# Optimization experiments

Hardware: AMD Instinct MI355X
Metric: run time of the kernel (lower is better)

Reference implementation:

```python
import jax, jax.numpy as jnp
import numpy as np

BN_EPS = 1e-5


def _edge_conv(x, W, b, gamma, beta, k):
    # x: [B, N, C_in]; W: [C_out, 2*C_in]
    inner = jnp.einsum('bnc,bmc->bnm', x, x)                 # [B,N,N]
    xx = jnp.sum(x * x, axis=-1)                             # [B,N]
    neg_dist = 2.0 * inner - xx[:, :, None] - xx[:, None, :]  # -||xi-xj||^2
    idx = jax.lax.top_k(neg_dist, k)[1]                      # [B,N,k]
    nbr = jax.vmap(lambda xb, ib: xb[ib])(x, idx)            # [B,N,k,C_in]
    ctr = x[:, :, None, :]                                   # [B,N,1,C_in]
    ef = jnp.concatenate([jnp.broadcast_to(ctr, nbr.shape), nbr - ctr], axis=-1)  # [B,N,k,2C]
    h = jnp.einsum('bnkc,oc->bnko', ef, W) + b               # 1x1 conv -> [B,N,k,C_out]
    # BatchNorm2d (training mode: biased batch stats over B,N,k)
    mean = jnp.mean(h, axis=(0, 1, 2))
    var = jnp.mean(jnp.square(h - mean), axis=(0, 1, 2))
    h = (h - mean) * jax.lax.rsqrt(var + BN_EPS) * gamma + beta
    h = jax.nn.relu(h)
    return jnp.max(h, axis=2)                                # max over k neighbors -> [B,N,C_out]


def setup_inputs() -> dict:
    key = jax.random.key(0)
    ks = jax.random.split(key, 8)
    B, N, IN = 8, 2048, 3
    dims = [64, 128, 256]
    inp = {'x': jax.random.normal(ks[0], (B, N, IN), dtype=jnp.float32)}
    prev = IN
    for i, d in enumerate(dims):
        kk = jax.random.fold_in(ks[1], i)
        inp[f'w{i+1}'] = jax.random.normal(kk, (d, 2 * prev), dtype=jnp.float32) * (1.0 / np.sqrt(2 * prev))
        inp[f'b{i+1}'] = jnp.zeros((d,), dtype=jnp.float32)
        inp[f'g{i+1}'] = jnp.ones((d,), dtype=jnp.float32)
        inp[f'be{i+1}'] = jnp.zeros((d,), dtype=jnp.float32)
        prev = d
    inp['wo'] = jax.random.normal(ks[2], (dims[-1], dims[-1]), dtype=jnp.float32) * (1.0 / np.sqrt(dims[-1]))
    inp['bo'] = jnp.zeros((dims[-1],), dtype=jnp.float32)
    inp['k'] = 20
    return inp


def reference(x, w1, b1, g1, be1, w2, b2, g2, be2, w3, b3, g3, be3, wo, bo, k):
    h = _edge_conv(x, w1, b1, g1, be1, k)
    h = _edge_conv(h, w2, b2, g2, be2, k)
    h = _edge_conv(h, w3, b3, g3, be3, k)
    h = jnp.max(h, axis=1)          # global max-pool over points -> [B, 256]
    return h @ wo.T + bo
```

## Files before the change

### kernel.cpp

```cpp
#include <hip/hip_runtime.h>
#include <cmath>

static constexpr int Bb  = 8;
static constexpr int Nn  = 2048;
static constexpr int KNB = 20;
static constexpr int NPT = Bb * Nn;
static constexpr int NTRI = 528;
#define EPSBN 1e-5f

__device__ __forceinline__ int permc(int c) { return c ^ (4 * (c >> 5)); }

__device__ __forceinline__ unsigned mkkey(float v) {
  unsigned u = __float_as_uint(v);
  return (u & 0x80000000u) ? ~u : (u | 0x80000000u);
}

__global__ __launch_bounds__(256) void row_sumsq_k(const float* __restrict__ f,
                                                   float* __restrict__ xx, int C) {
  int g = blockIdx.x * 256 + threadIdx.x;
  if (g >= NPT) return;
  const float* r = f + (size_t)g * C;
  float s = 0.f;
  if ((C & 3) == 0) {
    const float4* r4 = (const float4*)r;
    for (int j = 0; j < C / 4; ++j) {
      float4 v = r4[j];
      s += v.x * v.x + v.y * v.y + v.z * v.z + v.w * v.w;
    }
  } else {
    for (int j = 0; j < C; ++j) { float v = r[j]; s += v * v; }
  }
  xx[g] = s;
}

__global__ __launch_bounds__(256) void dist_k(const float* __restrict__ f,
                                              const float* __restrict__ xx,
                                              float* __restrict__ nd, int C) {
  __shared__ float As[16 * 68];
  __shared__ float Bs[16 * 68];
  float* Sc = As;
  int tid = threadIdx.x, tx = tid & 15, ty = tid >> 4;
  int b, p;
  if (gridDim.x == NTRI * Bb) { b = blockIdx.x & 7; p = blockIdx.x >> 3; }
  else                        { b = blockIdx.z;     p = blockIdx.x; }
  const float* fb  = f  + (size_t)b * Nn * C;
  const float* xxb = xx + (size_t)b * Nn;
  float* ndb = nd + (size_t)b * Nn * Nn;
  int rblk = 0;
  while (p >= 32 - rblk) { p -= 32 - rblk; ++rblk; }
  int rb = rblk * 64, cb = (rblk + p) * 64;
  bool diag = (rb == cb);
  int kk0 = tid & 15, rr = tid >> 4;
  float acc[4][4] = {};
  float pa[4], pb[4];
  {
    bool ok = kk0 < C;
    #pragma unroll
    for (int t = 0; t < 4; ++t) {
      int r2 = rr + 16 * t;
      pa[t] = ok ? fb[(size_t)(rb + r2) * C + kk0] : 0.f;
      pb[t] = ok ? fb[(size_t)(cb + r2) * C + kk0] : 0.f;
    }
  }
  for (int k0 = 0; k0 < C; k0 += 16) {
    __syncthreads();
    #pragma unroll
    for (int t = 0; t < 4; ++t) {
      int r2 = rr + 16 * t;
      As[kk0 * 68 + r2] = pa[t];
      Bs[kk0 * 68 + r2] = pb[t];
    }
    __syncthreads();
    if (k0 + 16 < C) {
      int k2 = k0 + 16 + kk0;
      bool ok2 = k2 < C;
      #pragma unroll
      for (int t = 0; t < 4; ++t) {
        int r2 = rr + 16 * t;
        pa[t] = ok2 ? fb[(size_t)(rb + r2) * C + k2] : 0.f;
        pb[t] = ok2 ? fb[(size_t)(cb + r2) * C + k2] : 0.f;
      }
    }
    #pragma unroll
    for (int kk = 0; kk < 16; ++kk) {
      float4 a4 = *(const float4*)&As[kk * 68 + 4 * ty];
      float4 b4 = *(const float4*)&Bs[kk * 68 + 4 * tx];
      float av[4] = {a4.x, a4.y, a4.z, a4.w};
      float bv[4] = {b4.x, b4.y, b4.z, b4.w};
      #pragma unroll
      for (int i = 0; i < 4; ++i)
        #pragma unroll
        for (int j = 0; j < 4; ++j) acc[i][j] += av[i] * bv[j];
    }
  }
  float xr[4], xc[4];
  #pragma unroll
  for (int i = 0; i < 4; ++i) xr[i] = xxb[rb + 4 * ty + i];
  #pragma unroll
  for (int j = 0; j < 4; ++j) xc[j] = xxb[cb + 4 * tx + j];
  #pragma unroll
  for (int i = 0; i < 4; ++i) {
    int grow = rb + 4 * ty + i;
    #pragma unroll
    for (int j = 0; j < 4; ++j) {
      int gcol = cb + 4 * tx + j;
      float v = 2.f * acc[i][j] - xr[i] - xc[j];
      acc[i][j] = (grow == gcol) ? 0.f : v;
    }
    *(float4*)&ndb[(size_t)grow * Nn + cb + 4 * tx] =
        make_float4(acc[i][0], acc[i][1], acc[i][2], acc[i][3]);
  }
  if (!diag) {
    int sRow = tid >> 4, c4 = tid & 15;
    #pragma unroll
    for (int h = 0; h < 4; ++h) {
      __syncthreads();
      if ((tx >> 2) == h) {
        int txl = tx & 3;
        #pragma unroll
        for (int j = 0; j < 4; ++j)
          *(float4*)&Sc[(4 * txl + j) * 68 + 4 * ty] =
              make_float4(acc[0][j], acc[1][j], acc[2][j], acc[3][j]);
      }
      __syncthreads();
      float4 v = *(const float4*)&Sc[sRow * 68 + 4 * c4];
      *(float4*)&ndb[(size_t)(cb + 16 * h + sRow) * Nn + rb + 4 * c4] = v;
    }
  }
}

__global__ __launch_bounds__(256) void topk_k(const float* __restrict__ nd,
                                              int* __restrict__ outidx) {
  __shared__ unsigned ck[Nn];
  __shared__ unsigned short ci[Nn];
  __shared__ unsigned Tw[4];
  __shared__ int s_cnt;
  int tid = threadIdx.x, lane = tid & 63;
  int n;
  if (gridDim.x == NPT) {
    int bb = blockIdx.x & 7, row = blockIdx.x >> 3;
    n = bb * Nn + row;
  } else {
    n = blockIdx.x;
  }
  const float4* rowp = (const float4*)(nd + (size_t)n * Nn);
  int* orow = outidx + (size_t)n * KNB;
  if (tid == 0) s_cnt = 0;
  float4 va = rowp[tid];
  float4 vb = rowp[tid + 256];
  unsigned k0 = mkkey(va.x), k1 = mkkey(va.y), k2 = mkkey(va.z), k3 = mkkey(va.w);
  unsigned k4 = mkkey(vb.x), k5 = mkkey(vb.y), k6 = mkkey(vb.z), k7 = mkkey(vb.w);
  unsigned t1 = k0;
  t1 = k1 > t1 ? k1 : t1; t1 = k2 > t1 ? k2 : t1; t1 = k3 > t1 ? k3 : t1;
  t1 = k4 > t1 ? k4 : t1; t1 = k5 > t1 ? k5 : t1; t1 = k6 > t1 ? k6 : t1;
  t1 = k7 > t1 ? k7 : t1;
  bool alive = true;
  unsigned wmax = 0;
  #pragma unroll
  for (int r = 0; r < 5; ++r) {
    unsigned v = alive ? t1 : 0u;
    wmax = v;
    #pragma unroll
    for (int off = 1; off < 64; off <<= 1) {
      unsigned o = (unsigned)__shfl_xor((int)wmax, off, 64);
      wmax = o > wmax ? o : wmax;
    }
    unsigned long long ball = __ballot(alive && t1 == wmax);
    int first = __ffsll((long long)ball) - 1;
    if (lane == first) alive = false;
  }
  if (lane == 0) Tw[tid >> 6] = wmax;
  __syncthreads();
  unsigned T = Tw[0];
  T = Tw[1] < T ? Tw[1] : T;
  T = Tw[2] < T ? Tw[2] : T;
  T = Tw[3] < T ? Tw[3] : T;
  int c0 = 4 * tid, c4 = 1024 + 4 * tid;
  if (k0 >= T) { int p2 = atomicAdd(&s_cnt, 1); ck[p2] = k0; ci[p2] = (unsigned short)(c0); }
  if (k1 >= T) { int p2 = atomicAdd(&s_cnt, 1); ck[p2] = k1; ci[p2] = (unsigned short)(c0 + 1); }
  if (k2 >= T) { int p2 = atomicAdd(&s_cnt, 1); ck[p2] = k2; ci[p2] = (unsigned short)(c0 + 2); }
  if (k3 >= T) { int p2 = atomicAdd(&s_cnt, 1); ck[p2] = k3; ci[p2] = (unsigned short)(c0 + 3); }
  if (k4 >= T) { int p2 = atomicAdd(&s_cnt, 1); ck[p2] = k4; ci[p2] = (unsigned short)(c4); }
  if (k5 >= T) { int p2 = atomicAdd(&s_cnt, 1); ck[p2] = k5; ci[p2] = (unsigned short)(c4 + 1); }
  if (k6 >= T) { int p2 = atomicAdd(&s_cnt, 1); ck[p2] = k6; ci[p2] = (unsigned short)(c4 + 2); }
  if (k7 >= T) { int p2 = atomicAdd(&s_cnt, 1); ck[p2] = k7; ci[p2] = (unsigned short)(c4 + 3); }
  __syncthreads();
  int nc = s_cnt;
  for (int j = tid; j < nc; j += 256) {
    unsigned kj = ck[j];
    unsigned ij = ci[j];
    int rank = 0;
    for (int i = 0; i < nc; ++i) {
      unsigned ki = ck[i];
      unsigned ii = ci[i];
      rank += (ki > kj || (ki == kj && ii < ij)) ? 1 : 0;
    }
    if (rank < KNB) orow[rank] = (int)ij;
  }
}

__global__ __launch_bounds__(256) void gemmAB_k(const float* __restrict__ X,
                                                const float* __restrict__ W,
                                                const float* __restrict__ bias,
                                                float* __restrict__ A,
                                                float* __restrict__ Bv,
                                                int COUT, int CIN) {
  __shared__ float Xs[16][132];
  __shared__ float Ws[16][132];
  int tid = threadIdx.x, tx = tid & 15, ty = tid >> 4;
  int mb = blockIdx.y * 128, cb = blockIdx.x * 128;
  int kk0 = tid & 15, rr = tid >> 4;
  int ldw = 2 * CIN;
  float acc[8][8] = {};
  for (int k0 = 0; k0 < CIN; k0 += 16) {
    int k = k0 + kk0;
    bool ok = k < CIN;
    #pragma unroll
    for (int r2 = rr; r2 < 128; r2 += 16) {
      Xs[kk0][permc(r2)] = ok ? X[(size_t)(mb + r2) * CIN + k] : 0.f;
      int c2 = cb + r2;
      const float* wr = (c2 < COUT) ? (W + (size_t)c2 * ldw)
                                    : (W + (size_t)(c2 - COUT) * ldw + CIN);
      Ws[kk0][permc(r2)] = ok ? wr[k] : 0.f;
    }
    __syncthreads();
    #pragma unroll
    for (int kk = 0; kk < 16; ++kk) {
      float4 a0 = *(const float4*)&Xs[kk][permc(8 * ty)];
      float4 a1 = *(const float4*)&Xs[kk][permc(8 * ty + 4)];
      float4 b0 = *(const float4*)&Ws[kk][permc(8 * tx)];
      float4 b1 = *(const float4*)&Ws[kk][permc(8 * tx + 4)];
      float av[8] = {a0.x, a0.y, a0.z, a0.w, a1.x, a1.y, a1.z, a1.w};
      float bv[8] = {b0.x, b0.y, b0.z, b0.w, b1.x, b1.y, b1.z, b1.w};
      #pragma unroll
      for (int i = 0; i < 8; ++i)
        #pragma unroll
        for (int j = 0; j < 8; ++j) acc[i][j] += av[i] * bv[j];
    }
    __syncthreads();
  }
  int c0 = cb + 8 * tx;
  bool isA = (c0 < COUT);
  float bb[8] = {0, 0, 0, 0, 0, 0, 0, 0};
  if (isA) {
    float4 b4a = *(const float4*)&bias[c0];
    float4 b4b = *(const float4*)&bias[c0 + 4];
    bb[0] = b4a.x; bb[1] = b4a.y; bb[2] = b4a.z; bb[3] = b4a.w;
    bb[4] = b4b.x; bb[5] = b4b.y; bb[6] = b4b.z; bb[7] = b4b.w;
  }
  float* dst = isA ? A : Bv;
  int cc = isA ? c0 : (c0 - COUT);
  #pragma unroll
  for (int i = 0; i < 8; ++i) {
    int m = mb + 8 * ty + i;
    *(float4*)&dst[(size_t)m * COUT + cc] =
        make_float4(acc[i][0] + bb[0], acc[i][1] + bb[1], acc[i][2] + bb[2], acc[i][3] + bb[3]);
    *(float4*)&dst[(size_t)m * COUT + cc + 4] =
        make_float4(acc[i][4] + bb[4], acc[i][5] + bb[5], acc[i][6] + bb[6], acc[i][7] + bb[7]);
  }
}

template <int COUT>
__global__ __launch_bounds__(256) void combine_k(const float* __restrict__ A,
                                                 const float* __restrict__ Bv,
                                                 const int* __restrict__ idx,
                                                 float* __restrict__ maxh,
                                                 float* __restrict__ minh,
                                                 float* __restrict__ gsum,
                                                 float* __restrict__ gsumsq) {
  constexpr int TPP = COUT / 4;
  constexpr int P = 256 / TPP;
  constexpr int PTS = 16;
  __shared__ float red[8][256];
  int tid = threadIdx.x;
  int p = tid / TPP, cq = tid % TPP;
  int b = blockIdx.x & 7, chunk = blockIdx.x >> 3;
  int nbase = b * Nn + chunk * PTS;
  const float4* A4 = (const float4*)A;
  const float4* B4 = (const float4*)Bv;
  float4 ts = make_float4(0, 0, 0, 0), ts2 = make_float4(0, 0, 0, 0);
  for (int it = 0; it < PTS / P; ++it) {
    int n = nbase + it * P + p;
    float4 a  = A4[(size_t)n * TPP + cq];
    float4 bc = B4[(size_t)n * TPP + cq];
    float4 base = make_float4(a.x - bc.x, a.y - bc.y, a.z - bc.z, a.w - bc.w);
    float4 mx = make_float4(-INFINITY, -INFINITY, -INFINITY, -INFINITY);
    float4 mn = make_float4(INFINITY, INFINITY, INFINITY, INFINITY);
    int gb = b * Nn;
    const int* ip = idx + (size_t)n * KNB;
    for (int k = 0; k < KNB; ++k) {
      int m = ip[k];
      float4 bn = B4[(size_t)(gb + m) * TPP + cq];
      float4 h = make_float4(base.x + bn.x, base.y + bn.y, base.z + bn.z, base.w + bn.w);
      mx.x = fmaxf(mx.x, h.x); mx.y = fmaxf(mx.y, h.y);
      mx.z = fmaxf(mx.z, h.z); mx.w = fmaxf(mx.w, h.w);
      mn.x = fminf(mn.x, h.x); mn.y = fminf(mn.y, h.y);
      mn.z = fminf(mn.z, h.z); mn.w = fminf(mn.w, h.w);
      ts.x += h.x; ts.y += h.y; ts.z += h.z; ts.w += h.w;
      ts2.x += h.x * h.x; ts2.y += h.y * h.y; ts2.z += h.z * h.z; ts2.w += h.w * h.w;
    }
    ((float4*)maxh)[(size_t)n * TPP + cq] = mx;
    ((float4*)minh)[(size_t)n * TPP + cq] = mn;
  }
  red[0][tid] = ts.x;  red[1][tid] = ts.y;  red[2][tid] = ts.z;  red[3][tid] = ts.w;
  red[4][tid] = ts2.x; red[5][tid] = ts2.y; red[6][tid] = ts2.z; red[7][tid] = ts2.w;
  __syncthreads();
  if (tid < COUT) {
    int q = tid & 3, g = tid >> 2;
    float s = 0.f, s2 = 0.f;
    for (int pp = 0; pp < P; ++pp) {
      int t2 = pp * TPP + g;
      s += red[q][t2]; s2 += red[4 + q][t2];
    }
    atomicAdd(&gsum[tid], s);
    atomicAdd(&gsumsq[tid], s2);
  }
}

__global__ void stats_k(const float* __restrict__ gsum, const float* __restrict__ gsumsq,
                        const float* __restrict__ gamma, const float* __restrict__ beta,
                        float* __restrict__ sA, float* __restrict__ sB, int COUT) {
  int c = threadIdx.x;
  if (c < COUT) {
    const float cnt = (float)((size_t)Bb * Nn * KNB);
    float mean = gsum[c] / cnt;
    float var = gsumsq[c] / cnt - mean * mean;
    var = fmaxf(var, 0.f);
    float s = gamma[c] * rsqrtf(var + EPSBN);
    sA[c] = s;
    sB[c] = beta[c] - mean * s;
  }
}

__global__ __launch_bounds__(256) void apply_k(const float* __restrict__ maxh,
                                               const float* __restrict__ minh,
                                               const float* __restrict__ sA,
                                               const float* __restrict__ sB,
                                               float* __restrict__ out, int COUT) {
  int i = blockIdx.x * 256 + threadIdx.x;
  if (i >= NPT * COUT) return;
  int c = i % COUT;
  float s = sA[c];
  float h = (s >= 0.f) ? maxh[i] : minh[i];
  out[i] = fmaxf(s * h + sB[c], 0.f);
}

__global__ __launch_bounds__(256) void gmax3_k(const float* __restrict__ maxh,
                                               const float* __restrict__ minh,
                                               const float* __restrict__ sA,
                                               const float* __restrict__ sB,
                                               unsigned* __restrict__ pooled) {
  int b = blockIdx.y, chunk = blockIdx.x;
  int c = threadIdx.x;
  float s = sA[c], t = sB[c];
  const float* src = (s >= 0.f) ? maxh : minh;
  const float* fb = src + ((size_t)b * Nn + chunk * 32) * 256;
  float m = 0.f;
  #pragma unroll 8
  for (int r = 0; r < 32; ++r) m = fmaxf(m, fmaxf(s * fb[(size_t)r * 256 + c] + t, 0.f));
  atomicMax(&pooled[b * 256 + c], __float_as_uint(m));
}

__global__ void final_k(const float* __restrict__ pooled, const float* __restrict__ wo,
                        const float* __restrict__ bo, float* __restrict__ out) {
  int b = blockIdx.x, c = threadIdx.x;
  const float* pr = pooled + b * 256;
  const float* wr = wo + c * 256;
  float s = bo[c];
  for (int j = 0; j < 256; ++j) s += pr[j] * wr[j];
  out[b * 256 + c] = s;
}

template <int CIN, int COUT, bool LAST>
static void run_layer(const float* fin, const float* W, const float* bias,
                      const float* gamma, const float* beta, float* fout,
                      float* nd, bool big, float* Abuf, float* Bvbuf, int* idxb,
                      float* xx, float* maxh, float* minh, float* gsum,
                      float* sA, float* sB, unsigned* pooled, hipStream_t stream) {
  row_sumsq_k<<<(NPT + 255) / 256, 256, 0, stream>>>(fin, xx, CIN);
  if (big) {
    dist_k<<<dim3(NTRI * Bb), 256, 0, stream>>>(fin, xx, nd, CIN);
    topk_k<<<NPT, 256, 0, stream>>>(nd, idxb);
  } else {
    for (int b = 0; b < Bb; ++b) {
      dist_k<<<dim3(NTRI, 1, 1), 256, 0, stream>>>(
          fin + (size_t)b * Nn * CIN, xx + (size_t)b * Nn, nd, CIN);
      topk_k<<<Nn, 256, 0, stream>>>(nd, idxb + (size_t)b * Nn * KNB);
    }
  }
  gemmAB_k<<<dim3(2 * COUT / 128, NPT / 128), 256, 0, stream>>>(fin, W, bias,
                                                                Abuf, Bvbuf, COUT, CIN);
  hipMemsetAsync(gsum, 0, 2 * 256 * sizeof(float), stream);
  combine_k<COUT><<<NPT / 16, 256, 0, stream>>>(Abuf, Bvbuf, idxb, maxh, minh,
                                                gsum, gsum + 256);
  stats_k<<<1, 256, 0, stream>>>(gsum, gsum + 256, gamma, beta, sA, sB, COUT);
  if (LAST) {
    gmax3_k<<<dim3(Nn / 32, Bb), 256, 0, stream>>>(maxh, minh, sA, sB, pooled);
  } else {
    apply_k<<<(NPT * COUT + 255) / 256, 256, 0, stream>>>(maxh, minh, sA, sB, fout, COUT);
  }
}

extern "C" void kernel_launch(void* const* d_in, const int* in_sizes, int n_in,
                              void* d_out, int out_size, void* d_ws, size_t ws_size,
                              hipStream_t stream) {
  const float* x   = (const float*)d_in[0];
  const float* w1  = (const float*)d_in[1];
  const float* b1  = (const float*)d_in[2];
  const float* g1  = (const float*)d_in[3];
  const float* be1 = (const float*)d_in[4];
  const float* w2  = (const float*)d_in[5];
  const float* b2  = (const float*)d_in[6];
  const float* g2  = (const float*)d_in[7];
  const float* be2 = (const float*)d_in[8];
  const float* w3  = (const float*)d_in[9];
  const float* b3  = (const float*)d_in[10];
  const float* g3  = (const float*)d_in[11];
  const float* be3 = (const float*)d_in[12];
  const float* wo  = (const float*)d_in[13];
  const float* bo  = (const float*)d_in[14];
  float* out = (float*)d_out;

  char* ws = (char*)d_ws;
  size_t off = 0;
  auto grab = [&](size_t bytes) -> char* {
    char* p = ws + off;
    off = (off + bytes + 255) & ~(size_t)255;
    return p;
  };
  const size_t SLAB = (size_t)NPT * 256 * 4;
  const size_t ND_ALL = (size_t)Bb * Nn * Nn * 4;
  const size_t NEED_BIG = ND_ALL + ((size_t)NPT * KNB * 4) + ((size_t)NPT * 4) +
                          ((size_t)NPT * 64 * 4) + ((size_t)NPT * 128 * 4) +
                          (16 << 10) + 16 * 256;
  bool big = (ws_size >= NEED_BIG);

  float *nd, *Abuf, *Bvbuf, *maxh, *minh;
  if (big) {
    nd    = (float*)grab(ND_ALL);
    Abuf  = nd;
    Bvbuf = (float*)((char*)nd + SLAB);
    maxh  = (float*)((char*)nd + 2 * SLAB);
    minh  = (float*)((char*)nd + 3 * SLAB);
  } else {
    nd    = (float*)grab((size_t)Nn * Nn * 4);
    Abuf  = nd;
    Bvbuf = (float*)grab(SLAB);
    maxh  = nullptr; minh = nullptr;
  }
  int*   idxb  = (int*)  grab((size_t)NPT * KNB * 4);
  float* xx    = (float*)grab((size_t)NPT * 4);
  float* feat1 = (float*)grab((size_t)NPT * 64 * 4);
  float* feat2 = (float*)grab((size_t)NPT * 128 * 4);
  if (!big) {
    maxh = (float*)grab(SLAB);
    minh = (float*)grab(SLAB);
  }
  float* gsum  = (float*)grab(2 * 256 * 4);
  float* sA    = (float*)grab(256 * 4);
  float* sB    = (float*)grab(256 * 4);
  unsigned* pooled = (unsigned*)grab(Bb * 256 * 4);

  hipMemsetAsync(pooled, 0, Bb * 256 * sizeof(unsigned), stream);

  run_layer<3, 64, false>(x, w1, b1, g1, be1, feat1, nd, big, Abuf, Bvbuf, idxb, xx,
                          maxh, minh, gsum, sA, sB, pooled, stream);
  run_layer<64, 128, false>(feat1, w2, b2, g2, be2, feat2, nd, big, Abuf, Bvbuf, idxb, xx,
                            maxh, minh, gsum, sA, sB, pooled, stream);
  run_layer<128, 256, true>(feat2, w3, b3, g3, be3, nullptr, nd, big, Abuf, Bvbuf, idxb, xx,
                            maxh, minh, gsum, sA, sB, pooled, stream);

  final_k<<<Bb, 256, 0, stream>>>((const float*)pooled, wo, bo, out);
  (void)in_sizes; (void)n_in; (void)out_size;
}
```

Measured before the change: 611.7 us.

## Skip mirrored distance writes; read lower triangle via column access in top-k

The distance kernel now writes only the upper-triangle tiles and no longer transposes them through shared memory to fill the mirrored half. The top-k kernel reconstructs each row by reading its own row from the diagonal tile onward and reading the missing part from the corresponding column, which uses strided loads. This removes half of the distance-matrix writes and the extra syncs, but the strided column reads are uncoalesced, and each thread's elements are now 8 contiguous entries instead of interleaved float4s.

```diff
diff --git a/kernel.cpp b/kernel.cpp
--- a/kernel.cpp
+++ b/kernel.cpp
@@ -38,7 +38,6 @@
                                               float* __restrict__ nd, int C) {
   __shared__ float As[16 * 68];
   __shared__ float Bs[16 * 68];
-  float* Sc = As;
   int tid = threadIdx.x, tx = tid & 15, ty = tid >> 4;
   int b, p;
   if (gridDim.x == NTRI * Bb) { b = blockIdx.x & 7; p = blockIdx.x >> 3; }
@@ -49,7 +48,6 @@
   int rblk = 0;
   while (p >= 32 - rblk) { p -= 32 - rblk; ++rblk; }
   int rb = rblk * 64, cb = (rblk + p) * 64;
-  bool diag = (rb == cb);
   int kk0 = tid & 15, rr = tid >> 4;
   float acc[4][4] = {};
   float pa[4], pb[4];
@@ -109,23 +107,6 @@
     }
     *(float4*)&ndb[(size_t)grow * Nn + cb + 4 * tx] =
         make_float4(acc[i][0], acc[i][1], acc[i][2], acc[i][3]);
-  }
-  if (!diag) {
-    int sRow = tid >> 4, c4 = tid & 15;
-    #pragma unroll
-    for (int h = 0; h < 4; ++h) {
-      __syncthreads();
-      if ((tx >> 2) == h) {
-        int txl = tx & 3;
-        #pragma unroll
-        for (int j = 0; j < 4; ++j)
-          *(float4*)&Sc[(4 * txl + j) * 68 + 4 * ty] =
-              make_float4(acc[0][j], acc[1][j], acc[2][j], acc[3][j]);
-      }
-      __syncthreads();
-      float4 v = *(const float4*)&Sc[sRow * 68 + 4 * c4];
-      *(float4*)&ndb[(size_t)(cb + 16 * h + sRow) * Nn + rb + 4 * c4] = v;
-    }
   }
 }
 
@@ -143,13 +124,26 @@
   } else {
     n = blockIdx.x;
   }
-  const float4* rowp = (const float4*)(nd + (size_t)n * Nn);
+  int rn = n & (Nn - 1);
+  size_t rowBase   = (size_t)n * Nn;
+  size_t batchBase = (size_t)(n - rn) * Nn;
+  int dStart = (rn >> 6) << 6;
   int* orow = outidx + (size_t)n * KNB;
   if (tid == 0) s_cnt = 0;
-  float4 va = rowp[tid];
-  float4 vb = rowp[tid + 256];
-  unsigned k0 = mkkey(va.x), k1 = mkkey(va.y), k2 = mkkey(va.z), k3 = mkkey(va.w);
-  unsigned k4 = mkkey(vb.x), k5 = mkkey(vb.y), k6 = mkkey(vb.z), k7 = mkkey(vb.w);
+  int mStart = 8 * tid;
+  unsigned k0, k1, k2, k3, k4, k5, k6, k7;
+  if (mStart >= dStart) {
+    const float4* dp = (const float4*)(nd + rowBase + mStart);
+    float4 va = dp[0], vb = dp[1];
+    k0 = mkkey(va.x); k1 = mkkey(va.y); k2 = mkkey(va.z); k3 = mkkey(va.w);
+    k4 = mkkey(vb.x); k5 = mkkey(vb.y); k6 = mkkey(vb.z); k7 = mkkey(vb.w);
+  } else {
+    const float* mp = nd + batchBase + (size_t)mStart * Nn + rn;
+    k0 = mkkey(mp[0]);        k1 = mkkey(mp[(size_t)Nn]);
+    k2 = mkkey(mp[2 * (size_t)Nn]); k3 = mkkey(mp[3 * (size_t)Nn]);
+    k4 = mkkey(mp[4 * (size_t)Nn]); k5 = mkkey(mp[5 * (size_t)Nn]);
+    k6 = mkkey(mp[6 * (size_t)Nn]); k7 = mkkey(mp[7 * (size_t)Nn]);
+  }
   unsigned t1 = k0;
   t1 = k1 > t1 ? k1 : t1; t1 = k2 > t1 ? k2 : t1; t1 = k3 > t1 ? k3 : t1;
   t1 = k4 > t1 ? k4 : t1; t1 = k5 > t1 ? k5 : t1; t1 = k6 > t1 ? k6 : t1;
@@ -175,15 +169,14 @@
   T = Tw[1] < T ? Tw[1] : T;
   T = Tw[2] < T ? Tw[2] : T;
   T = Tw[3] < T ? Tw[3] : T;
-  int c0 = 4 * tid, c4 = 1024 + 4 * tid;
-  if (k0 >= T) { int p2 = atomicAdd(&s_cnt, 1); ck[p2] = k0; ci[p2] = (unsigned short)(c0); }
-  if (k1 >= T) { int p2 = atomicAdd(&s_cnt, 1); ck[p2] = k1; ci[p2] = (unsigned short)(c0 + 1); }
-  if (k2 >= T) { int p2 = atomicAdd(&s_cnt, 1); ck[p2] = k2; ci[p2] = (unsigned short)(c0 + 2); }
-  if (k3 >= T) { int p2 = atomicAdd(&s_cnt, 1); ck[p2] = k3; ci[p2] = (unsigned short)(c0 + 3); }
-  if (k4 >= T) { int p2 = atomicAdd(&s_cnt, 1); ck[p2] = k4; ci[p2] = (unsigned short)(c4); }
-  if (k5 >= T) { int p2 = atomicAdd(&s_cnt, 1); ck[p2] = k5; ci[p2] = (unsigned short)(c4 + 1); }
-  if (k6 >= T) { int p2 = atomicAdd(&s_cnt, 1); ck[p2] = k6; ci[p2] = (unsigned short)(c4 + 2); }
-  if (k7 >= T) { int p2 = atomicAdd(&s_cnt, 1); ck[p2] = k7; ci[p2] = (unsigned short)(c4 + 3); }
+  if (k0 >= T) { int p2 = atomicAdd(&s_cnt, 1); ck[p2] = k0; ci[p2] = (unsigned short)(mStart); }
+  if (k1 >= T) { int p2 = atomicAdd(&s_cnt, 1); ck[p2] = k1; ci[p2] = (unsigned short)(mStart + 1); }
+  if (k2 >= T) { int p2 = atomicAdd(&s_cnt, 1); ck[p2] = k2; ci[p2] = (unsigned short)(mStart + 2); }
+  if (k3 >= T) { int p2 = atomicAdd(&s_cnt, 1); ck[p2] = k3; ci[p2] = (unsigned short)(mStart + 3); }
+  if (k4 >= T) { int p2 = atomicAdd(&s_cnt, 1); ck[p2] = k4; ci[p2] = (unsigned short)(mStart + 4); }
+  if (k5 >= T) { int p2 = atomicAdd(&s_cnt, 1); ck[p2] = k5; ci[p2] = (unsigned short)(mStart + 5); }
+  if (k6 >= T) { int p2 = atomicAdd(&s_cnt, 1); ck[p2] = k6; ci[p2] = (unsigned short)(mStart + 6); }
+  if (k7 >= T) { int p2 = atomicAdd(&s_cnt, 1); ck[p2] = k7; ci[p2] = (unsigned short)(mStart + 7); }
   __syncthreads();
   int nc = s_cnt;
   for (int j = tid; j < nc; j += 256) {
```

Result: slower. 691.1 us (+13.0%).
